# Performance work log

Measured on AMD Instinct MI355X. Metric: run time of the kernel, lower is better.

## Reference

```python
import jax, jax.numpy as jnp
import numpy as np


def setup_inputs() -> dict:
    key = jax.random.key(0)
    # Values near 1.0 so a 32k-long cumulative product neither under- nor overflows.
    x = jax.random.uniform(key, (4096, 32768), dtype=jnp.float32, minval=0.95, maxval=1.05)
    return {"x": x}


def reference(x):
    # Cumulative product along the last dim (module flattens to 2D, scans, reshapes back;
    # the flatten/reshape is a no-op mathematically for a last-dim scan).
    return jnp.cumprod(x, axis=-1)
```

## Files before the change

kernel.cpp:

```cpp
#include <hip/hip_runtime.h>


#define COLS   32768
#define TPB    256
#define WPB    (TPB / 64)
#define CHUNK  256
#define NPAIR  (COLS / (2 * CHUNK))
#define PFP    2

typedef float f32x4 __attribute__((ext_vector_type(4)));

#define ONE_BITS 0x3f800000

template <int CTRL, int RM, int BM>
__device__ __forceinline__ float mul_dpp(float x) {
    int s = __builtin_amdgcn_update_dpp(ONE_BITS, __float_as_int(x),
                                        CTRL, RM, BM, false);
    return x * __int_as_float(s);
}

__device__ __forceinline__ float wave_scan(float t) {
    t = mul_dpp<0x111, 0xf, 0xf>(t);
    t = mul_dpp<0x112, 0xf, 0xf>(t);
    t = mul_dpp<0x114, 0xf, 0xf>(t);
    t = mul_dpp<0x118, 0xf, 0xf>(t);
    t = mul_dpp<0x142, 0xa, 0xf>(t);
    t = mul_dpp<0x143, 0xc, 0xf>(t);
    return t;
}

__device__ __forceinline__ float excl(float t) {
    return __int_as_float(__builtin_amdgcn_update_dpp(
        ONE_BITS, __float_as_int(t), 0x138, 0xf, 0xf, false));
}

__global__ __launch_bounds__(TPB) void cumprod_rows(const float* __restrict__ x,
                                                    float* __restrict__ out) {
    const int lane = threadIdx.x & 63;
    const int wid  = threadIdx.x >> 6;
    const int row  = blockIdx.x * WPB + wid;

    const size_t base = (size_t)row * (size_t)COLS + (size_t)lane * 4;
    const float* px = x + base;
    float*       po = out + base;

    f32x4 buf[PFP][2];
    #pragma unroll
    for (int j = 0; j < PFP; ++j) {
        buf[j][0] = __builtin_nontemporal_load(
            reinterpret_cast<const f32x4*>(px + (2 * j)     * CHUNK));
        buf[j][1] = __builtin_nontemporal_load(
            reinterpret_cast<const f32x4*>(px + (2 * j + 1) * CHUNK));
    }

    float carry = 1.0f;

    for (int p = 0; p < NPAIR; p += PFP) {
        #pragma unroll
        for (int j = 0; j < PFP; ++j) {
            f32x4 vA = buf[j][0];
            f32x4 vB = buf[j][1];

            const int np = p + j + PFP;
            if (np < NPAIR) {
                buf[j][0] = __builtin_nontemporal_load(
                    reinterpret_cast<const f32x4*>(px + (2 * np)     * CHUNK));
                buf[j][1] = __builtin_nontemporal_load(
                    reinterpret_cast<const f32x4*>(px + (2 * np + 1) * CHUNK));
            }

            vA[1] *= vA[0]; vB[1] *= vB[0];
            vA[2] *= vA[1]; vB[2] *= vB[1];
            vA[3] *= vA[2]; vB[3] *= vB[2];

            float tA = wave_scan(vA[3]);
            float tB = wave_scan(vB[3]);
            float exA = excl(tA);
            float exB = excl(tB);

            float TA = __int_as_float(
                __builtin_amdgcn_readlane(__float_as_int(tA), 63));
            float TB = __int_as_float(
                __builtin_amdgcn_readlane(__float_as_int(tB), 63));
            const float mA = carry * exA;
            const float cA = carry * TA;
            const float mB = cA * exB;
            carry = cA * TB;

            f32x4 oA, oB;
            oA[0] = vA[0] * mA; oB[0] = vB[0] * mB;
            oA[1] = vA[1] * mA; oB[1] = vB[1] * mB;
            oA[2] = vA[2] * mA; oB[2] = vB[2] * mB;
            oA[3] = vA[3] * mA; oB[3] = vB[3] * mB;
            __builtin_nontemporal_store(oA,
                reinterpret_cast<f32x4*>(po + (2 * (p + j))     * CHUNK));
            __builtin_nontemporal_store(oB,
                reinterpret_cast<f32x4*>(po + (2 * (p + j) + 1) * CHUNK));
        }
    }
}

extern "C" void kernel_launch(void* const* d_in, const int* in_sizes, int n_in,
                              void* d_out, int out_size, void* d_ws, size_t ws_size,
                              hipStream_t stream) {
    const float* x = (const float*)d_in[0];
    float* out = (float*)d_out;
    const int rows = out_size / COLS;
    cumprod_rows<<<rows / WPB, TPB, 0, stream>>>(x, out);
}
```

Before: 212.5 us.

## Split rows into tiles with decoupled look-back scan across waves

Replaces the one-wave-per-row sequential scan with a decoupled look-back scan. Each wave handles a 2048-element tile of a row, taken in order via an atomic ticket, and publishes its aggregate and inclusive prefix to workspace. Later tiles spin on these values to get their carry. This gives much more parallelism and memory-level concurrency, since all of a tile's loads are issued up front. The cost is a memset, atomics, spin-waiting, and the assumption that a real product is never exactly 0.0, which is used as the not-ready flag. If the workspace is too small it falls back to the old kernel.

```diff
diff --git a/kernel.cpp b/kernel.cpp
--- a/kernel.cpp
+++ b/kernel.cpp
@@ -2,11 +2,12 @@
 
 
 #define COLS   32768
+#define CHUNK  256
+#define TCH    8
+#define TILE   (TCH * CHUNK)
+#define SEGS   (COLS / TILE)
 #define TPB    256
 #define WPB    (TPB / 64)
-#define CHUNK  256
-#define NPAIR  (COLS / (2 * CHUNK))
-#define PFP    2
 
 typedef float f32x4 __attribute__((ext_vector_type(4)));
 
@@ -34,12 +35,102 @@
         ONE_BITS, __float_as_int(t), 0x138, 0xf, 0xf, false));
 }
 
+__device__ __forceinline__ float read63(float t) {
+    return __int_as_float(__builtin_amdgcn_readlane(__float_as_int(t), 63));
+}
+
+__global__ __launch_bounds__(TPB) void cumprod_lookback(
+    const float* __restrict__ x, float* __restrict__ out,
+    unsigned* __restrict__ ticket_ctr,
+    float* __restrict__ agg, float* __restrict__ pref) {
+
+    __shared__ unsigned tk_s;
+    if (threadIdx.x == 0) tk_s = atomicAdd(ticket_ctr, 1u);
+    __syncthreads();
+
+    const int lane = threadIdx.x & 63;
+    const int wid  = threadIdx.x >> 6;
+    const unsigned tile = tk_s * WPB + wid;
+    const int row = tile >> 4;
+    const int seg = tile & (SEGS - 1);
+
+    const size_t base = (size_t)row * COLS + (size_t)seg * TILE + (size_t)lane * 4;
+    const float* px = x + base;
+    float*       po = out + base;
+
+    f32x4 buf[TCH];
+    #pragma unroll
+    for (int j = 0; j < TCH; ++j)
+        buf[j] = __builtin_nontemporal_load(
+            reinterpret_cast<const f32x4*>(px + j * CHUNK));
+
+    float carry = 1.0f;
+    #pragma unroll
+    for (int pq = 0; pq < TCH / 2; ++pq) {
+        f32x4 vA = buf[2 * pq], vB = buf[2 * pq + 1];
+        vA[1] *= vA[0]; vB[1] *= vB[0];
+        vA[2] *= vA[1]; vB[2] *= vB[1];
+        vA[3] *= vA[2]; vB[3] *= vB[2];
+        float tA = wave_scan(vA[3]);
+        float tB = wave_scan(vB[3]);
+        float exA = excl(tA), exB = excl(tB);
+        float TA = read63(tA), TB = read63(tB);
+        const float mA = carry * exA;
+        const float cA = carry * TA;
+        const float mB = cA * exB;
+        carry = cA * TB;
+        vA[0] *= mA; vA[1] *= mA; vA[2] *= mA; vA[3] *= mA;
+        vB[0] *= mB; vB[1] *= mB; vB[2] *= mB; vB[3] *= mB;
+        buf[2 * pq] = vA; buf[2 * pq + 1] = vB;
+    }
+
+    if (lane == 0)
+        __hip_atomic_store(&agg[tile], carry,
+                           __ATOMIC_RELAXED, __HIP_MEMORY_SCOPE_AGENT);
+
+    float p = 1.0f;
+    if (seg != 0) {
+        if (lane == 0) {
+            unsigned b = tile - 1;
+            const unsigned first = tile - seg;
+            for (;;) {
+                float pr = __hip_atomic_load(&pref[b],
+                    __ATOMIC_RELAXED, __HIP_MEMORY_SCOPE_AGENT);
+                if (pr != 0.0f) { p *= pr; break; }
+                float ag = __hip_atomic_load(&agg[b],
+                    __ATOMIC_RELAXED, __HIP_MEMORY_SCOPE_AGENT);
+                if (ag != 0.0f) {
+                    p *= ag;
+                    if (b == first) break;
+                    --b;
+                } else {
+                    __builtin_amdgcn_s_sleep(1);
+                }
+            }
+        }
+        p = __shfl(p, 0);
+    }
+
+    if (lane == 0 && seg != SEGS - 1)
+        __hip_atomic_store(&pref[tile], p * carry,
+                           __ATOMIC_RELAXED, __HIP_MEMORY_SCOPE_AGENT);
+
+    #pragma unroll
+    for (int j = 0; j < TCH; ++j) {
+        f32x4 o = buf[j];
+        o[0] *= p; o[1] *= p; o[2] *= p; o[3] *= p;
+        __builtin_nontemporal_store(o, reinterpret_cast<f32x4*>(po + j * CHUNK));
+    }
+}
+
+#define NPAIR (COLS / (2 * CHUNK))
+#define PFP   2
+
 __global__ __launch_bounds__(TPB) void cumprod_rows(const float* __restrict__ x,
                                                     float* __restrict__ out) {
     const int lane = threadIdx.x & 63;
     const int wid  = threadIdx.x >> 6;
     const int row  = blockIdx.x * WPB + wid;
-
     const size_t base = (size_t)row * (size_t)COLS + (size_t)lane * 4;
     const float* px = x + base;
     float*       po = out + base;
@@ -52,15 +143,11 @@
         buf[j][1] = __builtin_nontemporal_load(
             reinterpret_cast<const f32x4*>(px + (2 * j + 1) * CHUNK));
     }
-
     float carry = 1.0f;
-
     for (int p = 0; p < NPAIR; p += PFP) {
         #pragma unroll
         for (int j = 0; j < PFP; ++j) {
-            f32x4 vA = buf[j][0];
-            f32x4 vB = buf[j][1];
-
+            f32x4 vA = buf[j][0], vB = buf[j][1];
             const int np = p + j + PFP;
             if (np < NPAIR) {
                 buf[j][0] = __builtin_nontemporal_load(
@@ -68,25 +155,17 @@
                 buf[j][1] = __builtin_nontemporal_load(
                     reinterpret_cast<const f32x4*>(px + (2 * np + 1) * CHUNK));
             }
-
             vA[1] *= vA[0]; vB[1] *= vB[0];
             vA[2] *= vA[1]; vB[2] *= vB[1];
             vA[3] *= vA[2]; vB[3] *= vB[2];
-
             float tA = wave_scan(vA[3]);
             float tB = wave_scan(vB[3]);
-            float exA = excl(tA);
-            float exB = excl(tB);
-
-            float TA = __int_as_float(
-                __builtin_amdgcn_readlane(__float_as_int(tA), 63));
-            float TB = __int_as_float(
-                __builtin_amdgcn_readlane(__float_as_int(tB), 63));
+            float exA = excl(tA), exB = excl(tB);
+            float TA = read63(tA), TB = read63(tB);
             const float mA = carry * exA;
             const float cA = carry * TA;
             const float mB = cA * exB;
             carry = cA * TB;
-
             f32x4 oA, oB;
             oA[0] = vA[0] * mA; oB[0] = vB[0] * mB;
             oA[1] = vA[1] * mA; oB[1] = vB[1] * mB;
@@ -105,6 +184,17 @@
                               hipStream_t stream) {
     const float* x = (const float*)d_in[0];
     float* out = (float*)d_out;
-    const int rows = out_size / COLS;
-    cumprod_rows<<<rows / WPB, TPB, 0, stream>>>(x, out);
-}
+    const int rows   = out_size / COLS;
+    const int ntiles = rows * SEGS;
+
+    const size_t need = 64 + (size_t)ntiles * 4 * 2;
+    if (ws_size >= need) {
+        hipMemsetAsync(d_ws, 0, need, stream);
+        unsigned* ctr = (unsigned*)d_ws;
+        float* agg  = (float*)((char*)d_ws + 64);
+        float* pref = agg + ntiles;
+        cumprod_lookback<<<ntiles / WPB, TPB, 0, stream>>>(x, out, ctr, agg, pref);
+    } else {
+        cumprod_rows<<<rows / WPB, TPB, 0, stream>>>(x, out);
+    }
+}
```

After: 278.0 us. +30.8%, slower.

## Split each row across 16 waves with register-resident chunks and cross-wave carry scan

Applied to the files above, without the earlier changes.

Instead of one wave scanning a whole 32k row serially with a software prefetch pipeline, each 1024-thread block now handles one row. Each of its 16 waves loads its 2048-element segment into registers at once, scans it locally, and publishes its total to shared memory. An exclusive cross-wave product then fixes up each segment before it is stored. This aims to expose far more memory-level parallelism and shorten the serial carry chain per wave, at the cost of a block barrier and higher register use per thread.

```diff
diff --git a/kernel.cpp b/kernel.cpp
--- a/kernel.cpp
+++ b/kernel.cpp
@@ -1,12 +1,12 @@
 #include <hip/hip_runtime.h>
 
 
-#define COLS   32768
-#define TPB    256
-#define WPB    (TPB / 64)
-#define CHUNK  256
-#define NPAIR  (COLS / (2 * CHUNK))
-#define PFP    2
+#define COLS  32768
+#define TPB   1024
+#define NW    (TPB / 64)
+#define PERW  (COLS / NW)
+#define TCH   8
+#define CHUNK 256
 
 typedef float f32x4 __attribute__((ext_vector_type(4)));
 
@@ -34,69 +34,64 @@
         ONE_BITS, __float_as_int(t), 0x138, 0xf, 0xf, false));
 }
 
-__global__ __launch_bounds__(TPB) void cumprod_rows(const float* __restrict__ x,
-                                                    float* __restrict__ out) {
+__device__ __forceinline__ float read63(float t) {
+    return __int_as_float(__builtin_amdgcn_readlane(__float_as_int(t), 63));
+}
+
+__global__ __launch_bounds__(TPB, 8) void cumprod_rows(
+    const float* __restrict__ x, float* __restrict__ out) {
+
     const int lane = threadIdx.x & 63;
     const int wid  = threadIdx.x >> 6;
-    const int row  = blockIdx.x * WPB + wid;
 
-    const size_t base = (size_t)row * (size_t)COLS + (size_t)lane * 4;
+    const size_t base = (size_t)blockIdx.x * COLS
+                      + (size_t)wid * PERW + (size_t)lane * 4;
     const float* px = x + base;
     float*       po = out + base;
 
-    f32x4 buf[PFP][2];
+    f32x4 buf[TCH];
     #pragma unroll
-    for (int j = 0; j < PFP; ++j) {
-        buf[j][0] = __builtin_nontemporal_load(
-            reinterpret_cast<const f32x4*>(px + (2 * j)     * CHUNK));
-        buf[j][1] = __builtin_nontemporal_load(
-            reinterpret_cast<const f32x4*>(px + (2 * j + 1) * CHUNK));
+    for (int j = 0; j < TCH; ++j)
+        buf[j] = __builtin_nontemporal_load(
+            reinterpret_cast<const f32x4*>(px + j * CHUNK));
+
+    float carry = 1.0f;
+    #pragma unroll
+    for (int pq = 0; pq < TCH / 2; ++pq) {
+        f32x4 vA = buf[2 * pq], vB = buf[2 * pq + 1];
+        vA[1] *= vA[0]; vB[1] *= vB[0];
+        vA[2] *= vA[1]; vB[2] *= vB[1];
+        vA[3] *= vA[2]; vB[3] *= vB[2];
+        float tA = wave_scan(vA[3]);
+        float tB = wave_scan(vB[3]);
+        float exA = excl(tA), exB = excl(tB);
+        float TA = read63(tA), TB = read63(tB);
+        const float mA = carry * exA;
+        const float cA = carry * TA;
+        const float mB = cA * exB;
+        carry = cA * TB;
+        vA[0] *= mA; vA[1] *= mA; vA[2] *= mA; vA[3] *= mA;
+        vB[0] *= mB; vB[1] *= mB; vB[2] *= mB; vB[3] *= mB;
+        buf[2 * pq] = vA; buf[2 * pq + 1] = vB;
     }
 
-    float carry = 1.0f;
+    __shared__ float wt[NW];
+    if (lane == 0) wt[wid] = carry;
+    __syncthreads();
 
-    for (int p = 0; p < NPAIR; p += PFP) {
-        #pragma unroll
-        for (int j = 0; j < PFP; ++j) {
-            f32x4 vA = buf[j][0];
-            f32x4 vB = buf[j][1];
+    float v = 1.0f;
+    if (lane < wid) v = wt[lane];
+    v *= __shfl_xor(v, 1);
+    v *= __shfl_xor(v, 2);
+    v *= __shfl_xor(v, 4);
+    v *= __shfl_xor(v, 8);
+    const float p = __shfl(v, 0);
 
-            const int np = p + j + PFP;
-            if (np < NPAIR) {
-                buf[j][0] = __builtin_nontemporal_load(
-                    reinterpret_cast<const f32x4*>(px + (2 * np)     * CHUNK));
-                buf[j][1] = __builtin_nontemporal_load(
-                    reinterpret_cast<const f32x4*>(px + (2 * np + 1) * CHUNK));
-            }
-
-            vA[1] *= vA[0]; vB[1] *= vB[0];
-            vA[2] *= vA[1]; vB[2] *= vB[1];
-            vA[3] *= vA[2]; vB[3] *= vB[2];
-
-            float tA = wave_scan(vA[3]);
-            float tB = wave_scan(vB[3]);
-            float exA = excl(tA);
-            float exB = excl(tB);
-
-            float TA = __int_as_float(
-                __builtin_amdgcn_readlane(__float_as_int(tA), 63));
-            float TB = __int_as_float(
-                __builtin_amdgcn_readlane(__float_as_int(tB), 63));
-            const float mA = carry * exA;
-            const float cA = carry * TA;
-            const float mB = cA * exB;
-            carry = cA * TB;
-
-            f32x4 oA, oB;
-            oA[0] = vA[0] * mA; oB[0] = vB[0] * mB;
-            oA[1] = vA[1] * mA; oB[1] = vB[1] * mB;
-            oA[2] = vA[2] * mA; oB[2] = vB[2] * mB;
-            oA[3] = vA[3] * mA; oB[3] = vB[3] * mB;
-            __builtin_nontemporal_store(oA,
-                reinterpret_cast<f32x4*>(po + (2 * (p + j))     * CHUNK));
-            __builtin_nontemporal_store(oB,
-                reinterpret_cast<f32x4*>(po + (2 * (p + j) + 1) * CHUNK));
-        }
+    #pragma unroll
+    for (int j = 0; j < TCH; ++j) {
+        f32x4 o = buf[j];
+        o[0] *= p; o[1] *= p; o[2] *= p; o[3] *= p;
+        __builtin_nontemporal_store(o, reinterpret_cast<f32x4*>(po + j * CHUNK));
     }
 }
 
@@ -106,5 +101,5 @@
     const float* x = (const float*)d_in[0];
     float* out = (float*)d_out;
     const int rows = out_size / COLS;
-    cumprod_rows<<<rows / WPB, TPB, 0, stream>>>(x, out);
+    cumprod_rows<<<rows, TPB, 0, stream>>>(x, out);
 }
```

Measured after the change: 190.7 us. 10.3% less time.
